# Kernel tuning notes

Hardware: AMD Instinct MI355X
Metric: run time of the kernel (lower is better)

## Reference

```python
import jax, jax.numpy as jnp
import numpy as np

N_NODES = 100000
N_EDGES = 1600000
IN_DIM = 128
HEADS = 2
OUT_DIM = 64


def setup_inputs() -> dict:
    key = jax.random.key(0)
    k1, k2, k3, k4, k5 = jax.random.split(key, 5)
    x = jax.random.normal(k1, (N_NODES, IN_DIM), dtype=jnp.float32)
    edge_index = jax.random.randint(k2, (2, N_EDGES), 0, N_NODES, dtype=jnp.int32)
    # xavier-uniform-ish scales
    W = jax.random.uniform(k3, (IN_DIM, HEADS * OUT_DIM), dtype=jnp.float32,
                           minval=-1.0, maxval=1.0) * (6.0 / (IN_DIM + HEADS * OUT_DIM)) ** 0.5
    attn_l = jax.random.uniform(k4, (HEADS, OUT_DIM), dtype=jnp.float32,
                                minval=-1.0, maxval=1.0) * (6.0 / (HEADS + OUT_DIM)) ** 0.5
    attn_r = jax.random.uniform(k5, (HEADS, OUT_DIM), dtype=jnp.float32,
                                minval=-1.0, maxval=1.0) * (6.0 / (HEADS + OUT_DIM)) ** 0.5
    return {"x": x, "edge_index": edge_index, "W": W, "attn_l": attn_l, "attn_r": attn_r}


def reference(x, edge_index, W, attn_l, attn_r):
    N = x.shape[0]
    h = (x @ W).reshape(N, HEADS, OUT_DIM)          # [N,H,D]
    src, dst = edge_index[0], edge_index[1]          # [E]
    h_src = h[src]                                   # [E,H,D] gather
    h_dst = h[dst]                                   # [E,H,D] gather
    # per-edge, per-head attention logits
    alpha = jnp.einsum('ehd,hd->eh', h_src, attn_l) + jnp.einsum('ehd,hd->eh', h_dst, attn_r)
    alpha = jax.nn.leaky_relu(alpha, negative_slope=0.2)
    # NOTE: faithful to original torch code: softmax over dim=0 (ALL edges per head)
    alpha = jax.nn.softmax(alpha, axis=0)            # [E,H]
    msg = h_src * alpha[:, :, None]                  # [E,H,D]
    out = jnp.zeros((N, HEADS, OUT_DIM), dtype=h.dtype).at[dst].add(msg)
    return out.reshape(N, HEADS * OUT_DIM)
```

## Files before the change

kernel.cpp:

```cpp
#include <hip/hip_runtime.h>
#include <hip/hip_fp16.h>
#include <math.h>

#define IN_DIM   128
#define HEADS    2
#define OUT_DIM  64
#define OCOLS    128
#define NB_A     1024
#define BSHIFT   8
#define MAXB     512
#define PCOPIES  8
#define CAP      6144
#define PARTB    128
#define LOG2E    1.4426950408889634f

typedef __attribute__((ext_vector_type(4))) _Float16 half4v;
typedef __attribute__((ext_vector_type(8))) _Float16 half8v;
typedef __attribute__((ext_vector_type(4))) float    floatx4;

__global__ __launch_bounds__(256) void pack_w_kernel(
    const float* __restrict__ W, half8v* __restrict__ wpack) {
  int t = threadIdx.x;
  for (int s = t; s < 2048; s += 256) {
    int l = s & 63, ct = (s >> 6) & 7, kk = s >> 9;
    int q = l >> 4, n = l & 15;
    int c = ct * 16 + n;
    half8v f;
#pragma unroll
    for (int j = 0; j < 8; j++) {
      f[j] = (_Float16)W[(size_t)(kk * 32 + q * 8 + j) * OCOLS + c];
    }
    wpack[s] = f;
  }
}

__global__ __launch_bounds__(256) void gemm_kernel(
    const float* __restrict__ x, const half8v* __restrict__ wpack,
    const float* __restrict__ attn_l, const float* __restrict__ attn_r,
    _Float16* __restrict__ h16, float* __restrict__ alr, int N) {
  __shared__ half8v Wlds[2048];
  __shared__ __align__(16) _Float16 hstage[64 * OCOLS];
  const int tid = threadIdx.x;
  for (int i = tid; i < 2048; i += 256) Wlds[i] = wpack[i];

  const int wave = tid >> 6, lane = tid & 63;
  const int q = lane >> 4, m = lane & 15;
  const int rbase = blockIdx.x * 64 + wave * 16;
  const int arow = rbase + m;
  const bool rok = arow < N;

  half8v a[4];
#pragma unroll
  for (int kk = 0; kk < 4; kk++) {
    float4 u = rok ? *(const float4*)&x[(size_t)arow * IN_DIM + kk * 32 + q * 8]
                   : make_float4(0.f, 0.f, 0.f, 0.f);
    float4 v = rok ? *(const float4*)&x[(size_t)arow * IN_DIM + kk * 32 + q * 8 + 4]
                   : make_float4(0.f, 0.f, 0.f, 0.f);
    a[kk][0] = (_Float16)u.x; a[kk][1] = (_Float16)u.y;
    a[kk][2] = (_Float16)u.z; a[kk][3] = (_Float16)u.w;
    a[kk][4] = (_Float16)v.x; a[kk][5] = (_Float16)v.y;
    a[kk][6] = (_Float16)v.z; a[kk][7] = (_Float16)v.w;
  }
  __syncthreads();

  floatx4 acc[8];
#pragma unroll
  for (int ct = 0; ct < 8; ct++) {
    floatx4 c = {0.f, 0.f, 0.f, 0.f};
#pragma unroll
    for (int kk = 0; kk < 4; kk++) {
      c = __builtin_amdgcn_mfma_f32_16x16x32_f16(
          a[kk], Wlds[(kk * 8 + ct) * 64 + lane], c, 0, 0, 0);
    }
    acc[ct] = c;
  }

  float Al[8], Ar[8];
#pragma unroll
  for (int ct = 0; ct < 8; ct++) {
    Al[ct] = attn_l[ct * 16 + m];
    Ar[ct] = attn_r[ct * 16 + m];
  }
#pragma unroll
  for (int r = 0; r < 4; r++) {
    float al0 = 0.f, al1 = 0.f, ar0 = 0.f, ar1 = 0.f;
#pragma unroll
    for (int ct = 0; ct < 4; ct++) {
      al0 += acc[ct][r] * Al[ct];
      ar0 += acc[ct][r] * Ar[ct];
      al1 += acc[ct + 4][r] * Al[ct + 4];
      ar1 += acc[ct + 4][r] * Ar[ct + 4];
    }
#pragma unroll
    for (int off = 1; off < 16; off <<= 1) {
      al0 += __shfl_xor(al0, off);
      al1 += __shfl_xor(al1, off);
      ar0 += __shfl_xor(ar0, off);
      ar1 += __shfl_xor(ar1, off);
    }
    int orow = rbase + q * 4 + r;
    if (m == 0 && orow < N) {
      *(float4*)&alr[(size_t)orow * 4] =
          make_float4(al0 * LOG2E, al1 * LOG2E, ar0 * LOG2E, ar1 * LOG2E);
    }
  }

#pragma unroll
  for (int ct = 0; ct < 8; ct++) {
#pragma unroll
    for (int r = 0; r < 4; r++) {
      hstage[(wave * 16 + q * 4 + r) * OCOLS + ct * 16 + m] = (_Float16)acc[ct][r];
    }
  }
  __syncthreads();
  {
    int srow = tid >> 2, seg = tid & 3;
    int grow = blockIdx.x * 64 + srow;
    if (grow < N) {
      const int4* s = (const int4*)&hstage[srow * OCOLS + seg * 32];
      int4* d = (int4*)&h16[(size_t)grow * OCOLS + seg * 32];
      int4 v0 = s[0], v1 = s[1], v2 = s[2], v3 = s[3];
      d[0] = v0; d[1] = v1; d[2] = v2; d[3] = v3;
    }
  }
}

__device__ inline void softmax_comb(float& m, float& s, float m2, float s2) {
  float M = fmaxf(m, m2);
  s = s * __builtin_amdgcn_exp2f(m - M) + s2 * __builtin_amdgcn_exp2f(m2 - M);
  m = M;
}

__global__ __launch_bounds__(256) void alpha_stats_kernel(
    const int* __restrict__ src, const int* __restrict__ dst,
    const float* __restrict__ alr, float* __restrict__ partials,
    int* __restrict__ bucket_cnt, int E, int nb1) {
  __shared__ int hist[MAXB];
  for (int i = threadIdx.x; i < MAXB; i += 256) hist[i] = 0;
  __syncthreads();
  const char* ab = (const char*)alr;
  float m0 = -1e30f, s0 = 0.f, m1 = -1e30f, s1 = 0.f;
  for (int e = blockIdx.x * 256 + threadIdx.x; e < E; e += gridDim.x * 256) {
    int sn = src[e], dn = dst[e];
    atomicAdd(&hist[dn >> BSHIFT], 1);
    float4 as = *(const float4*)(ab + ((unsigned)sn << 4));
    float4 ad = *(const float4*)(ab + ((unsigned)dn << 4));
    float a0 = as.x + ad.z;
    float a1 = as.y + ad.w;
    a0 = (a0 > 0.f) ? a0 : 0.2f * a0;
    a1 = (a1 > 0.f) ? a1 : 0.2f * a1;
    {
      float M = fmaxf(m0, a0);
      s0 = s0 * __builtin_amdgcn_exp2f(m0 - M) + __builtin_amdgcn_exp2f(a0 - M);
      m0 = M;
    }
    {
      float M = fmaxf(m1, a1);
      s1 = s1 * __builtin_amdgcn_exp2f(m1 - M) + __builtin_amdgcn_exp2f(a1 - M);
      m1 = M;
    }
  }
  __syncthreads();
  for (int b = threadIdx.x; b < nb1; b += 256) {
    int h = hist[b];
    if (h) atomicAdd(&bucket_cnt[(blockIdx.x & (PCOPIES - 1)) * MAXB + b], h);
  }
#pragma unroll
  for (int off = 1; off < 64; off <<= 1) {
    float m0o = __shfl_xor(m0, off), s0o = __shfl_xor(s0, off);
    float m1o = __shfl_xor(m1, off), s1o = __shfl_xor(s1, off);
    softmax_comb(m0, s0, m0o, s0o);
    softmax_comb(m1, s1, m1o, s1o);
  }
  __shared__ float red[4][4];
  int wave = threadIdx.x >> 6;
  int lane = threadIdx.x & 63;
  if (lane == 0) {
    red[wave][0] = m0; red[wave][1] = s0; red[wave][2] = m1; red[wave][3] = s1;
  }
  __syncthreads();
  if (threadIdx.x == 0) {
    float M0 = red[0][0], S0 = red[0][1], M1 = red[0][2], S1 = red[0][3];
    for (int w = 1; w < 4; w++) {
      softmax_comb(M0, S0, red[w][0], red[w][1]);
      softmax_comb(M1, S1, red[w][2], red[w][3]);
    }
    float* p = &partials[(size_t)blockIdx.x * 4];
    p[0] = M0; p[1] = S0; p[2] = M1; p[3] = S1;
  }
}

__global__ __launch_bounds__(256) void reduce_kernel(
    const float* __restrict__ partials, float* __restrict__ stats) {
  float m0 = -1e30f, s0 = 0.f, m1 = -1e30f, s1 = 0.f;
  for (int i = threadIdx.x; i < NB_A; i += 256) {
    const float* p = &partials[(size_t)i * 4];
    softmax_comb(m0, s0, p[0], p[1]);
    softmax_comb(m1, s1, p[2], p[3]);
  }
#pragma unroll
  for (int off = 1; off < 64; off <<= 1) {
    float m0o = __shfl_xor(m0, off), s0o = __shfl_xor(s0, off);
    float m1o = __shfl_xor(m1, off), s1o = __shfl_xor(s1, off);
    softmax_comb(m0, s0, m0o, s0o);
    softmax_comb(m1, s1, m1o, s1o);
  }
  __shared__ float red[4][4];
  int wave = threadIdx.x >> 6;
  int lane = threadIdx.x & 63;
  if (lane == 0) {
    red[wave][0] = m0; red[wave][1] = s0; red[wave][2] = m1; red[wave][3] = s1;
  }
  __syncthreads();
  if (threadIdx.x == 0) {
    float M0 = red[0][0], S0 = red[0][1], M1 = red[0][2], S1 = red[0][3];
    for (int w = 1; w < 4; w++) {
      softmax_comb(M0, S0, red[w][0], red[w][1]);
      softmax_comb(M1, S1, red[w][2], red[w][3]);
    }
    stats[0] = M0; stats[1] = 1.f / S0;
    stats[2] = M1; stats[3] = 1.f / S1;
  }
}

__global__ __launch_bounds__(512) void bucket_scan_kernel(
    const int* __restrict__ bucket_cnt, int* __restrict__ bucket_off,
    int* __restrict__ bucket_cursor, int nb1) {
  __shared__ int part[512];
  int t = threadIdx.x;
  int v = 0;
  if (t < nb1) {
#pragma unroll
    for (int c = 0; c < PCOPIES; c++) v += bucket_cnt[c * MAXB + t];
  }
  part[t] = v;
  __syncthreads();
  for (int d = 1; d < 512; d <<= 1) {
    int x = (t >= d) ? part[t - d] : 0;
    __syncthreads();
    part[t] += x;
    __syncthreads();
  }
  int excl = part[t] - v;
  if (t < nb1) {
    bucket_off[t] = excl;
    bucket_cursor[t] = excl;
  }
  if (t == 511) bucket_off[nb1] = part[511];
}

__global__ __launch_bounds__(256) void partition_kernel(
    const int* __restrict__ src, const int* __restrict__ dst,
    int* __restrict__ bucket_cursor, unsigned int* __restrict__ pairs,
    int E, int nb1, int chunk) {
  __shared__ int hist[MAXB];
  __shared__ int cur[MAXB];
  int base = blockIdx.x * chunk;
  int lim = min(base + chunk, E);
  for (int i = threadIdx.x; i < MAXB; i += 256) hist[i] = 0;
  __syncthreads();
  for (int e = base + threadIdx.x; e < lim; e += 256) {
    atomicAdd(&hist[dst[e] >> BSHIFT], 1);
  }
  __syncthreads();
  for (int b = threadIdx.x; b < nb1; b += 256) {
    cur[b] = atomicAdd(&bucket_cursor[b], hist[b]);
  }
  __syncthreads();
  for (int e = base + threadIdx.x; e < lim; e += 256) {
    int d = dst[e];
    int slot = atomicAdd(&cur[d >> BSHIFT], 1);
    pairs[slot] = (unsigned int)src[e] | ((unsigned int)(d & 255) << 17);
  }
}

__global__ __launch_bounds__(256) void bucket_csr_kernel(
    const unsigned int* __restrict__ pairs, const int* __restrict__ bucket_off,
    int* __restrict__ off, int* __restrict__ edge_src, int N, int nb1) {
  __shared__ int hist[256];
  __shared__ int cur[256];
  __shared__ int buf[CAP];
  int b = blockIdx.x;
  int t = threadIdx.x;
  int base_node = b << BSHIFT;
  int nn = min(256, N - base_node);
  int pbeg = bucket_off[b], pend = bucket_off[b + 1];
  int cntE = pend - pbeg;

  hist[t] = 0;
  __syncthreads();
  for (int i = t; i < cntE; i += 256) {
    atomicAdd(&hist[pairs[pbeg + i] >> 17], 1);
  }
  __syncthreads();
  int v = hist[t];
  for (int d = 1; d < 256; d <<= 1) {
    int x = (t >= d) ? hist[t - d] : 0;
    __syncthreads();
    hist[t] += x;
    __syncthreads();
  }
  int excl = hist[t] - v;
  cur[t] = excl;
  if (t < nn) off[base_node + t] = pbeg + excl;
  if (b == nb1 - 1 && t == 0) off[N] = pend;
  __syncthreads();
  if (cntE <= CAP) {
    for (int i = t; i < cntE; i += 256) {
      unsigned int p = pairs[pbeg + i];
      int slot = atomicAdd(&cur[p >> 17], 1);
      buf[slot] = (int)(p & 0x1FFFFu);
    }
    __syncthreads();
    for (int i = t; i < cntE; i += 256) {
      edge_src[pbeg + i] = buf[i];
    }
  } else {
    for (int i = t; i < cntE; i += 256) {
      unsigned int p = pairs[pbeg + i];
      int slot = atomicAdd(&cur[p >> 17], 1);
      edge_src[pbeg + slot] = (int)(p & 0x1FFFFu);
    }
  }
}

__global__ __launch_bounds__(256) void gather_kernel(
    const int* __restrict__ off, const int* __restrict__ edge_src,
    const float* __restrict__ alr, const float* __restrict__ stats,
    const _Float16* __restrict__ h16, float* __restrict__ out, int N) {
  int gid = blockIdx.x * 256 + threadIdx.x;
  int n = gid >> 6;
  if (n >= N) return;
  int lane = threadIdx.x & 63;
  int sub = lane >> 4;
  int l = lane & 15;
  int head = l >> 3;

  const char* ab = (const char*)alr;
  const char* hb = (const char*)h16;
  float4 ad = *(const float4*)(ab + ((unsigned)n << 4));
  float adv = head ? ad.w : ad.z;
  float M = stats[head * 2];
  float invS = stats[head * 2 + 1];
  unsigned loff = (unsigned)l * 16u;

  int beg = off[n], end = off[n + 1];
  float acc[8] = {0.f, 0.f, 0.f, 0.f, 0.f, 0.f, 0.f, 0.f};
  int i = beg + sub;
  for (; i + 4 < end; i += 8) {
    int sn0 = edge_src[i], sn1 = edge_src[i + 4];
    float4 as0 = *(const float4*)(ab + ((unsigned)sn0 << 4));
    float4 as1 = *(const float4*)(ab + ((unsigned)sn1 << 4));
    half8v hv0 = *(const half8v*)(hb + (((unsigned)sn0 << 8) + loff));
    half8v hv1 = *(const half8v*)(hb + (((unsigned)sn1 << 8) + loff));
    float a0 = (head ? as0.y : as0.x) + adv;
    float a1 = (head ? as1.y : as1.x) + adv;
    a0 = (a0 > 0.f) ? a0 : 0.2f * a0;
    a1 = (a1 > 0.f) ? a1 : 0.2f * a1;
    float w0 = __builtin_amdgcn_exp2f(a0 - M) * invS;
    float w1 = __builtin_amdgcn_exp2f(a1 - M) * invS;
#pragma unroll
    for (int j = 0; j < 8; j++) acc[j] += w0 * (float)hv0[j];
#pragma unroll
    for (int j = 0; j < 8; j++) acc[j] += w1 * (float)hv1[j];
  }
  if (i < end) {
    int sn = edge_src[i];
    float4 as = *(const float4*)(ab + ((unsigned)sn << 4));
    half8v hv = *(const half8v*)(hb + (((unsigned)sn << 8) + loff));
    float a = (head ? as.y : as.x) + adv;
    a = (a > 0.f) ? a : 0.2f * a;
    float w = __builtin_amdgcn_exp2f(a - M) * invS;
#pragma unroll
    for (int j = 0; j < 8; j++) acc[j] += w * (float)hv[j];
  }
#pragma unroll
  for (int j = 0; j < 8; j++) {
    acc[j] += __shfl_xor(acc[j], 16);
    acc[j] += __shfl_xor(acc[j], 32);
  }
  if (sub == 0) {
    char* ob = (char*)out;
    unsigned obase = ((unsigned)n << 9) + (unsigned)l * 32u;
    *(float4*)(ob + obase)      = make_float4(acc[0], acc[1], acc[2], acc[3]);
    *(float4*)(ob + obase + 16) = make_float4(acc[4], acc[5], acc[6], acc[7]);
  }
}

extern "C" void kernel_launch(void* const* d_in, const int* in_sizes, int n_in,
                              void* d_out, int out_size, void* d_ws, size_t ws_size,
                              hipStream_t stream) {
  const float* x      = (const float*)d_in[0];
  const int*   edge   = (const int*)d_in[1];
  const float* W      = (const float*)d_in[2];
  const float* attn_l = (const float*)d_in[3];
  const float* attn_r = (const float*)d_in[4];

  const int N = in_sizes[0] / IN_DIM;
  const int E = in_sizes[1] / 2;
  const int* src = edge;
  const int* dst = edge + E;
  float* out = (float*)d_out;

  const int nb1 = (N + 255) >> BSHIFT;

  _Float16*     h16      = (_Float16*)d_ws;
  float*        alr      = (float*)(h16 + (size_t)N * OCOLS);
  float*        partials = alr + (size_t)N * 4;
  float*        stats    = partials + (size_t)NB_A * 4;
  int*          bucket_cnt    = (int*)(stats + 4);
  int*          bucket_off    = bucket_cnt + PCOPIES * MAXB;
  int*          bucket_cursor = bucket_off + MAXB + 1;
  int*          off      = bucket_cursor + MAXB;
  unsigned int* pairs    = (unsigned int*)(off + N + 1);
  int*          edge_src = (int*)(pairs + E);
  half8v*       wpack    = (half8v*)(edge_src + E);

  const int chunk = (E + PARTB - 1) / PARTB;

  hipMemsetAsync(bucket_cnt, 0, PCOPIES * MAXB * sizeof(int), stream);

  pack_w_kernel<<<1, 256, 0, stream>>>(W, wpack);
  gemm_kernel<<<(N + 63) / 64, 256, 0, stream>>>(x, wpack, attn_l, attn_r, h16, alr, N);
  alpha_stats_kernel<<<NB_A, 256, 0, stream>>>(src, dst, alr, partials, bucket_cnt, E, nb1);
  reduce_kernel<<<1, 256, 0, stream>>>(partials, stats);
  bucket_scan_kernel<<<1, 512, 0, stream>>>(bucket_cnt, bucket_off, bucket_cursor, nb1);
  partition_kernel<<<PARTB, 256, 0, stream>>>(src, dst, bucket_cursor, pairs, E, nb1, chunk);
  bucket_csr_kernel<<<nb1, 256, 0, stream>>>(pairs, bucket_off, off, edge_src, N, nb1);
  gather_kernel<<<((size_t)N * 64 + 255) / 256, 256, 0, stream>>>(
      off, edge_src, alr, stats, h16, out, N);
}
```

Baseline: 283.4 us.

## Merge softmax reduce into bucket scan, widen partition grid, unroll gather with nontemporal access

Folds the single-block softmax statistics reduction into the bucket-scan launch as a second block, removing one kernel launch. Raises the partition grid from 128 to 512 blocks for more parallelism. The gather loop is unrolled to process four edges per sub-lane per iteration, raising memory-level parallelism. Edge-index loads and output stores become nontemporal to reduce cache pollution. The wider partition grid may increase atomic contention on the bucket cursors.

```diff
diff --git a/kernel.cpp b/kernel.cpp
--- a/kernel.cpp
+++ b/kernel.cpp
@@ -11,7 +11,7 @@
 #define MAXB     512
 #define PCOPIES  8
 #define CAP      6144
-#define PARTB    128
+#define PARTB    512
 #define LOG2E    1.4426950408889634f
 
 typedef __attribute__((ext_vector_type(4))) _Float16 half4v;
@@ -190,44 +190,45 @@
   }
 }
 
-__global__ __launch_bounds__(256) void reduce_kernel(
-    const float* __restrict__ partials, float* __restrict__ stats) {
-  float m0 = -1e30f, s0 = 0.f, m1 = -1e30f, s1 = 0.f;
-  for (int i = threadIdx.x; i < NB_A; i += 256) {
-    const float* p = &partials[(size_t)i * 4];
-    softmax_comb(m0, s0, p[0], p[1]);
-    softmax_comb(m1, s1, p[2], p[3]);
-  }
-#pragma unroll
-  for (int off = 1; off < 64; off <<= 1) {
-    float m0o = __shfl_xor(m0, off), s0o = __shfl_xor(s0, off);
-    float m1o = __shfl_xor(m1, off), s1o = __shfl_xor(s1, off);
-    softmax_comb(m0, s0, m0o, s0o);
-    softmax_comb(m1, s1, m1o, s1o);
-  }
-  __shared__ float red[4][4];
-  int wave = threadIdx.x >> 6;
-  int lane = threadIdx.x & 63;
-  if (lane == 0) {
-    red[wave][0] = m0; red[wave][1] = s0; red[wave][2] = m1; red[wave][3] = s1;
-  }
-  __syncthreads();
-  if (threadIdx.x == 0) {
-    float M0 = red[0][0], S0 = red[0][1], M1 = red[0][2], S1 = red[0][3];
-    for (int w = 1; w < 4; w++) {
-      softmax_comb(M0, S0, red[w][0], red[w][1]);
-      softmax_comb(M1, S1, red[w][2], red[w][3]);
-    }
-    stats[0] = M0; stats[1] = 1.f / S0;
-    stats[2] = M1; stats[3] = 1.f / S1;
-  }
-}
-
 __global__ __launch_bounds__(512) void bucket_scan_kernel(
     const int* __restrict__ bucket_cnt, int* __restrict__ bucket_off,
-    int* __restrict__ bucket_cursor, int nb1) {
+    int* __restrict__ bucket_cursor, const float* __restrict__ partials,
+    float* __restrict__ stats, int nb1) {
   __shared__ int part[512];
+  __shared__ float red[8][4];
   int t = threadIdx.x;
+
+  if (blockIdx.x == 1) {
+    float m0 = -1e30f, s0 = 0.f, m1 = -1e30f, s1 = 0.f;
+    for (int i = t; i < NB_A; i += 512) {
+      const float* p = &partials[(size_t)i * 4];
+      softmax_comb(m0, s0, p[0], p[1]);
+      softmax_comb(m1, s1, p[2], p[3]);
+    }
+#pragma unroll
+    for (int off = 1; off < 64; off <<= 1) {
+      float m0o = __shfl_xor(m0, off), s0o = __shfl_xor(s0, off);
+      float m1o = __shfl_xor(m1, off), s1o = __shfl_xor(s1, off);
+      softmax_comb(m0, s0, m0o, s0o);
+      softmax_comb(m1, s1, m1o, s1o);
+    }
+    int wave = t >> 6, lane = t & 63;
+    if (lane == 0) {
+      red[wave][0] = m0; red[wave][1] = s0; red[wave][2] = m1; red[wave][3] = s1;
+    }
+    __syncthreads();
+    if (t == 0) {
+      float M0 = red[0][0], S0 = red[0][1], M1 = red[0][2], S1 = red[0][3];
+      for (int w = 1; w < 8; w++) {
+        softmax_comb(M0, S0, red[w][0], red[w][1]);
+        softmax_comb(M1, S1, red[w][2], red[w][3]);
+      }
+      stats[0] = M0; stats[1] = 1.f / S0;
+      stats[2] = M1; stats[3] = 1.f / S1;
+    }
+    return;
+  }
+
   int v = 0;
   if (t < nb1) {
 #pragma unroll
@@ -347,8 +348,43 @@
   int beg = off[n], end = off[n + 1];
   float acc[8] = {0.f, 0.f, 0.f, 0.f, 0.f, 0.f, 0.f, 0.f};
   int i = beg + sub;
+  for (; i + 12 < end; i += 16) {
+    int sn0 = __builtin_nontemporal_load(&edge_src[i]);
+    int sn1 = __builtin_nontemporal_load(&edge_src[i + 4]);
+    int sn2 = __builtin_nontemporal_load(&edge_src[i + 8]);
+    int sn3 = __builtin_nontemporal_load(&edge_src[i + 12]);
+    float4 as0 = *(const float4*)(ab + ((unsigned)sn0 << 4));
+    float4 as1 = *(const float4*)(ab + ((unsigned)sn1 << 4));
+    float4 as2 = *(const float4*)(ab + ((unsigned)sn2 << 4));
+    float4 as3 = *(const float4*)(ab + ((unsigned)sn3 << 4));
+    half8v hv0 = *(const half8v*)(hb + (((unsigned)sn0 << 8) + loff));
+    half8v hv1 = *(const half8v*)(hb + (((unsigned)sn1 << 8) + loff));
+    half8v hv2 = *(const half8v*)(hb + (((unsigned)sn2 << 8) + loff));
+    half8v hv3 = *(const half8v*)(hb + (((unsigned)sn3 << 8) + loff));
+    float a0 = (head ? as0.y : as0.x) + adv;
+    float a1 = (head ? as1.y : as1.x) + adv;
+    float a2 = (head ? as2.y : as2.x) + adv;
+    float a3 = (head ? as3.y : as3.x) + adv;
+    a0 = (a0 > 0.f) ? a0 : 0.2f * a0;
+    a1 = (a1 > 0.f) ? a1 : 0.2f * a1;
+    a2 = (a2 > 0.f) ? a2 : 0.2f * a2;
+    a3 = (a3 > 0.f) ? a3 : 0.2f * a3;
+    float w0 = __builtin_amdgcn_exp2f(a0 - M) * invS;
+    float w1 = __builtin_amdgcn_exp2f(a1 - M) * invS;
+    float w2 = __builtin_amdgcn_exp2f(a2 - M) * invS;
+    float w3 = __builtin_amdgcn_exp2f(a3 - M) * invS;
+#pragma unroll
+    for (int j = 0; j < 8; j++) acc[j] += w0 * (float)hv0[j];
+#pragma unroll
+    for (int j = 0; j < 8; j++) acc[j] += w1 * (float)hv1[j];
+#pragma unroll
+    for (int j = 0; j < 8; j++) acc[j] += w2 * (float)hv2[j];
+#pragma unroll
+    for (int j = 0; j < 8; j++) acc[j] += w3 * (float)hv3[j];
+  }
   for (; i + 4 < end; i += 8) {
-    int sn0 = edge_src[i], sn1 = edge_src[i + 4];
+    int sn0 = __builtin_nontemporal_load(&edge_src[i]);
+    int sn1 = __builtin_nontemporal_load(&edge_src[i + 4]);
     float4 as0 = *(const float4*)(ab + ((unsigned)sn0 << 4));
     float4 as1 = *(const float4*)(ab + ((unsigned)sn1 << 4));
     half8v hv0 = *(const half8v*)(hb + (((unsigned)sn0 << 8) + loff));
@@ -365,7 +401,7 @@
     for (int j = 0; j < 8; j++) acc[j] += w1 * (float)hv1[j];
   }
   if (i < end) {
-    int sn = edge_src[i];
+    int sn = __builtin_nontemporal_load(&edge_src[i]);
     float4 as = *(const float4*)(ab + ((unsigned)sn << 4));
     half8v hv = *(const half8v*)(hb + (((unsigned)sn << 8) + loff));
     float a = (head ? as.y : as.x) + adv;
@@ -382,8 +418,10 @@
   if (sub == 0) {
     char* ob = (char*)out;
     unsigned obase = ((unsigned)n << 9) + (unsigned)l * 32u;
-    *(float4*)(ob + obase)      = make_float4(acc[0], acc[1], acc[2], acc[3]);
-    *(float4*)(ob + obase + 16) = make_float4(acc[4], acc[5], acc[6], acc[7]);
+    floatx4 o0 = {acc[0], acc[1], acc[2], acc[3]};
+    floatx4 o1 = {acc[4], acc[5], acc[6], acc[7]};
+    __builtin_nontemporal_store(o0, (floatx4*)(ob + obase));
+    __builtin_nontemporal_store(o1, (floatx4*)(ob + obase + 16));
   }
 }
 
@@ -423,8 +461,8 @@
   pack_w_kernel<<<1, 256, 0, stream>>>(W, wpack);
   gemm_kernel<<<(N + 63) / 64, 256, 0, stream>>>(x, wpack, attn_l, attn_r, h16, alr, N);
   alpha_stats_kernel<<<NB_A, 256, 0, stream>>>(src, dst, alr, partials, bucket_cnt, E, nb1);
-  reduce_kernel<<<1, 256, 0, stream>>>(partials, stats);
-  bucket_scan_kernel<<<1, 512, 0, stream>>>(bucket_cnt, bucket_off, bucket_cursor, nb1);
+  bucket_scan_kernel<<<2, 512, 0, stream>>>(bucket_cnt, bucket_off, bucket_cursor,
+                                            partials, stats, nb1);
   partition_kernel<<<PARTB, 256, 0, stream>>>(src, dst, bucket_cursor, pairs, E, nb1, chunk);
   bucket_csr_kernel<<<nb1, 256, 0, stream>>>(pairs, bucket_off, off, edge_src, N, nb1);
   gather_kernel<<<((size_t)N * 64 + 255) / 256, 256, 0, stream>>>(
```

New measurement: 270.9 us. 4.4% less time.
